# Kernel optimization log

Hardware: AMD Instinct MI355X
Metric: run time of the kernel (lower is better)

The kernel has to match this reference:

```python
import jax, jax.numpy as jnp
import numpy as np

N_HEADS = 16
HEAD_DIM = 64
HIDDEN = 1024


def setup_inputs() -> dict:
    key = jax.random.key(0)
    kx, kq, kk, kv, ko = jax.random.split(key, 5)
    B, S = 1, 4096
    # xavier_uniform for Linear(hidden, n_heads*head_dim): limit = sqrt(6/(fan_in+fan_out))
    lim = float(np.sqrt(6.0 / (HIDDEN + N_HEADS * HEAD_DIM)))
    x = jax.random.normal(kx, (B, S, HIDDEN), dtype=jnp.float32)
    wq = jax.random.uniform(kq, (N_HEADS * HEAD_DIM, HIDDEN), jnp.float32, -lim, lim)
    wk = jax.random.uniform(kk, (N_HEADS * HEAD_DIM, HIDDEN), jnp.float32, -lim, lim)
    wv = jax.random.uniform(kv, (N_HEADS * HEAD_DIM, HIDDEN), jnp.float32, -lim, lim)
    wo = jax.random.uniform(ko, (HIDDEN, N_HEADS * HEAD_DIM), jnp.float32, -lim, lim)
    return {"x": x, "wq": wq, "wk": wk, "wv": wv, "wo": wo}


def reference(x, wq, wk, wv, wo):
    B, S, _ = x.shape
    scale = HEAD_DIM ** -0.5
    # project and split heads: [B, H, S, D]
    def proj(w):
        return jnp.einsum('bsh,eh->bse', x, w).reshape(B, S, N_HEADS, HEAD_DIM).transpose(0, 2, 1, 3)
    q, k, v = proj(wq), proj(wk), proj(wv)
    scores = jnp.einsum('bhqd,bhkd->bhqk', q, k) * scale  # [B,H,S,S]
    causal = jnp.tril(jnp.ones((S, S), dtype=bool))
    scores = jnp.where(causal, scores, -jnp.inf)
    probs = jax.nn.softmax(scores, axis=-1)
    out = jnp.einsum('bhqk,bhkd->bhqd', probs, v)  # [B,H,S,D]
    out = out.transpose(0, 2, 1, 3).reshape(B, S, N_HEADS * HEAD_DIM)
    return jnp.einsum('bse,he->bsh', out, wo)
```

## Files before the change

### kernel.cpp

```cpp
#include <hip/hip_runtime.h>
#include <hip/hip_bf16.h>
#include <stdint.h>

typedef unsigned short u16;
typedef float f32x4 __attribute__((ext_vector_type(4)));
typedef __bf16 bf16x8 __attribute__((ext_vector_type(8)));
typedef u16 u16x8 __attribute__((ext_vector_type(8)));

#define GL2LDS16(g, l)                                                          \
  __builtin_amdgcn_global_load_lds(                                             \
      (const __attribute__((address_space(1))) unsigned int*)(g),               \
      (__attribute__((address_space(3))) unsigned int*)(l), 16, 0, 0)

#if __has_builtin(__builtin_amdgcn_exp2f)
#define EXP2(x) __builtin_amdgcn_exp2f(x)
#else
#define EXP2(x) exp2f(x)
#endif

#define SOFTMAX_SC 0.18033688f

__device__ __forceinline__ u16 f2bf(float f) {
  uint32_t u = __builtin_bit_cast(uint32_t, f);
  return (u16)((u + 0x7FFFu + ((u >> 16) & 1u)) >> 16);
}

__device__ __forceinline__ uint32_t cvt_pk_bf16(float lo, float hi) {
  uint32_t r;
  asm("v_cvt_pk_bf16_f32 %0, %1, %2" : "=v"(r) : "v"(lo), "v"(hi));
  return r;
}

__device__ __forceinline__ void cast8(const float* __restrict__ s,
                                      u16* __restrict__ d) {
  const float4* p = (const float4*)s;
  float4 a = p[0], b = p[1];
  uint4 o;
  o.x = cvt_pk_bf16(a.x, a.y);
  o.y = cvt_pk_bf16(a.z, a.w);
  o.z = cvt_pk_bf16(b.x, b.y);
  o.w = cvt_pk_bf16(b.z, b.w);
  *(uint4*)d = o;
}

__global__ __launch_bounds__(256) void cast_kernel(const float* __restrict__ s,
                                                   u16* __restrict__ d, int n) {
  int i = (blockIdx.x * 256 + threadIdx.x) * 8;
  if (i >= n) return;
  cast8(s + i, d + i);
}

__global__ __launch_bounds__(256) void cast4_kernel(const float* __restrict__ s0,
                                                    const float* __restrict__ s1,
                                                    const float* __restrict__ s2,
                                                    const float* __restrict__ s3,
                                                    u16* __restrict__ d) {
  int b = blockIdx.x >> 9;
  int i = ((blockIdx.x & 511) * 256 + threadIdx.x) * 8;
  const float* s = (b == 0) ? s0 : (b == 1) ? s1 : (b == 2) ? s2 : s3;
  cast8(s + i, d + ((size_t)b << 20) + i);
}

template <int MB>
__device__ __forceinline__ void mfma16(f32x4 (&acc)[8][4], const bf16x8 (&af)[4],
                                       const bf16x8 (&bfr)[4]) {
  asm volatile("s_waitcnt lgkmcnt(0)" ::: "memory");
  __builtin_amdgcn_sched_barrier(0);
  __builtin_amdgcn_s_setprio(1);
#pragma unroll
  for (int j = 0; j < 4; ++j)
#pragma unroll
    for (int n = 0; n < 4; ++n)
      acc[MB + j][n] = __builtin_amdgcn_mfma_f32_16x16x32_bf16(
          af[j], bfr[n], acc[MB + j][n], 0, 0, 0);
  __builtin_amdgcn_s_setprio(0);
}

__global__ __launch_bounds__(512, 2) void gemm8k(const u16* __restrict__ A,
                                                 const u16* __restrict__ B,
                                                 u16* __restrict__ C, int M,
                                                 int N, int K, int scaleq) {
  __shared__ u16 As[4][128 * 64];
  __shared__ u16 Bs[4][128 * 64];
  const int tid = threadIdx.x;
  const int lane = tid & 63;
  const int l15 = lane & 15, lhi = lane >> 4;
  const int wave = tid >> 6;
  const int wm = wave >> 2, wn = wave & 3;
  int bid = blockIdx.y * gridDim.x + blockIdx.x;
  const int cpx = (gridDim.x * gridDim.y) >> 3;
  bid = (bid & 7) * cpx + (bid >> 3);
  const int m0 = (bid / gridDim.x) * 256, n0 = (bid % gridDim.x) * 256;
  const int nt = K >> 6;

  int aoff[2][8], boff[2][4];
#pragma unroll
  for (int ks = 0; ks < 2; ++ks) {
    const int sl = ((ks * 4 + lhi) ^ (l15 & 7)) << 4;
#pragma unroll
    for (int m = 0; m < 8; ++m) aoff[ks][m] = (m * 16 + l15) * 128 + sl;
#pragma unroll
    for (int n = 0; n < 4; ++n)
      boff[ks][n] = ((wn & 1) * 64 + n * 16 + l15) * 128 + sl;
  }

  auto stA = [&](int T, int h) {
    u16* lb = As[(T & 1) * 2 + h];
#pragma unroll
    for (int i = 0; i < 2; ++i) {
      int c = tid + i * 512;
      int row = c >> 3;
      int scol = ((c & 7) ^ (row & 7)) * 8;
      GL2LDS16(A + (size_t)(m0 + h * 128 + row) * K + T * 64 + scol,
               (char*)lb + c * 16);
    }
  };
  auto stB = [&](int T, int h) {
    u16* lb = Bs[(T & 1) * 2 + h];
#pragma unroll
    for (int i = 0; i < 2; ++i) {
      int c = tid + i * 512;
      int row = c >> 3;
      int scol = ((c & 7) ^ (row & 7)) * 8;
      GL2LDS16(B + (size_t)(n0 + h * 128 + row) * K + T * 64 + scol,
               (char*)lb + c * 16);
    }
  };

  f32x4 acc[8][4] = {};

  stA(0, 0); stA(0, 1); stB(0, 0); stB(0, 1);
  asm volatile("s_waitcnt vmcnt(0)" ::: "memory");
  __builtin_amdgcn_s_barrier();

  for (int i = 0; i < nt / 2; ++i) {
    const int e = 2 * i, o = e + 1;
    const char* Ae = (const char*)As[wm];
    const char* Be = (const char*)Bs[wn >> 1];
    const char* Ao = (const char*)As[2 + wm];
    const char* Bo = (const char*)Bs[2 + (wn >> 1)];
    bf16x8 af[4], bfr[4];
    const bool pre = (e + 2) < nt;

    stA(o, 0); stA(o, 1);
    asm volatile("s_waitcnt vmcnt(4)" ::: "memory");
    __builtin_amdgcn_s_barrier();
#pragma unroll
    for (int j = 0; j < 4; ++j) af[j] = *(const bf16x8*)(Ae + aoff[0][j]);
#pragma unroll
    for (int n = 0; n < 4; ++n) bfr[n] = *(const bf16x8*)(Be + boff[0][n]);
    mfma16<0>(acc, af, bfr);
    __builtin_amdgcn_s_barrier();
#pragma unroll
    for (int j = 0; j < 4; ++j) af[j] = *(const bf16x8*)(Ae + aoff[0][4 + j]);
    stB(o, 0); stB(o, 1);
    __builtin_amdgcn_s_barrier();
    mfma16<4>(acc, af, bfr);
    __builtin_amdgcn_s_barrier();
#pragma unroll
    for (int j = 0; j < 4; ++j) af[j] = *(const bf16x8*)(Ae + aoff[1][j]);
#pragma unroll
    for (int n = 0; n < 4; ++n) bfr[n] = *(const bf16x8*)(Be + boff[1][n]);
    __builtin_amdgcn_s_barrier();
    mfma16<0>(acc, af, bfr);
    __builtin_amdgcn_s_barrier();
#pragma unroll
    for (int j = 0; j < 4; ++j) af[j] = *(const bf16x8*)(Ae + aoff[1][4 + j]);
    __builtin_amdgcn_s_barrier();
    mfma16<4>(acc, af, bfr);
    __builtin_amdgcn_s_barrier();
    if (pre) {
      stA(e + 2, 0); stA(e + 2, 1);
      asm volatile("s_waitcnt vmcnt(4)" ::: "memory");
    } else {
      asm volatile("s_waitcnt vmcnt(0)" ::: "memory");
    }
    __builtin_amdgcn_s_barrier();
#pragma unroll
    for (int j = 0; j < 4; ++j) af[j] = *(const bf16x8*)(Ao + aoff[0][j]);
#pragma unroll
    for (int n = 0; n < 4; ++n) bfr[n] = *(const bf16x8*)(Bo + boff[0][n]);
    mfma16<0>(acc, af, bfr);
    __builtin_amdgcn_s_barrier();
#pragma unroll
    for (int j = 0; j < 4; ++j) af[j] = *(const bf16x8*)(Ao + aoff[0][4 + j]);
    if (pre) { stB(e + 2, 0); stB(e + 2, 1); }
    __builtin_amdgcn_s_barrier();
    mfma16<4>(acc, af, bfr);
    __builtin_amdgcn_s_barrier();
#pragma unroll
    for (int j = 0; j < 4; ++j) af[j] = *(const bf16x8*)(Ao + aoff[1][j]);
#pragma unroll
    for (int n = 0; n < 4; ++n) bfr[n] = *(const bf16x8*)(Bo + boff[1][n]);
    __builtin_amdgcn_s_barrier();
    mfma16<0>(acc, af, bfr);
    __builtin_amdgcn_s_barrier();
#pragma unroll
    for (int j = 0; j < 4; ++j) af[j] = *(const bf16x8*)(Ao + aoff[1][4 + j]);
    __builtin_amdgcn_s_barrier();
    mfma16<4>(acc, af, bfr);
    __builtin_amdgcn_s_barrier();
  }

#pragma unroll
  for (int m = 0; m < 8; ++m) {
    int rbase = m0 + wm * 128 + m * 16 + lhi * 4;
#pragma unroll
    for (int n = 0; n < 4; ++n) {
      int col = n0 + wn * 64 + n * 16 + l15;
      float sc = (scaleq && col < 1024) ? SOFTMAX_SC : 1.0f;
#pragma unroll
      for (int r = 0; r < 4; ++r)
        C[(size_t)(rbase + r) * N + col] = f2bf(acc[m][n][r] * sc);
    }
  }
}

template <typename CT>
__global__ __launch_bounds__(256) void gemm_bt(const u16* __restrict__ A,
                                               const u16* __restrict__ B,
                                               CT* __restrict__ C, int M, int N,
                                               int K) {
  __shared__ u16 As[128 * 32];
  __shared__ u16 Bs[128 * 32];
  const int tid = threadIdx.x;
  const int lane = tid & 63;
  const int l15 = lane & 15, lhi = lane >> 4;
  const int wave = tid >> 6;
  const int wr = (wave >> 1) * 64, wc = (wave & 1) * 64;
  const int m0 = blockIdx.y * 128, n0 = blockIdx.x * 128;

  f32x4 acc[4][4] = {};

  for (int k0 = 0; k0 < K; k0 += 32) {
    __syncthreads();
#pragma unroll
    for (int i = 0; i < 2; ++i) {
      int c = tid + i * 256;
      int row = c >> 2, slot = c & 3;
      int scol = (slot ^ ((row >> 1) & 3)) * 8;
      GL2LDS16(A + (size_t)(m0 + row) * K + k0 + scol, (char*)As + c * 16);
      GL2LDS16(B + (size_t)(n0 + row) * K + k0 + scol, (char*)Bs + c * 16);
    }
    __syncthreads();
    bf16x8 af[4], bfr[4];
#pragma unroll
    for (int mi = 0; mi < 4; ++mi) {
      int row = wr + mi * 16 + l15;
      int byt = row * 64 + ((lhi ^ ((row >> 1) & 3)) << 4);
      af[mi] = *(const bf16x8*)((const char*)As + byt);
    }
#pragma unroll
    for (int ni = 0; ni < 4; ++ni) {
      int row = wc + ni * 16 + l15;
      int byt = row * 64 + ((lhi ^ ((row >> 1) & 3)) << 4);
      bfr[ni] = *(const bf16x8*)((const char*)Bs + byt);
    }
#pragma unroll
    for (int mi = 0; mi < 4; ++mi)
#pragma unroll
      for (int ni = 0; ni < 4; ++ni)
        acc[mi][ni] = __builtin_amdgcn_mfma_f32_16x16x32_bf16(
            af[mi], bfr[ni], acc[mi][ni], 0, 0, 0);
  }

#pragma unroll
  for (int mi = 0; mi < 4; ++mi) {
    int rbase = m0 + wr + mi * 16 + lhi * 4;
#pragma unroll
    for (int ni = 0; ni < 4; ++ni) {
      int col = n0 + wc + ni * 16 + l15;
#pragma unroll
      for (int r = 0; r < 4; ++r) {
        float v = acc[mi][ni][r];
        if constexpr (sizeof(CT) == 2)
          C[(size_t)(rbase + r) * N + col] = (CT)f2bf(v);
        else
          C[(size_t)(rbase + r) * N + col] = v;
      }
    }
  }
}

__global__ __launch_bounds__(256) void vtrans_kernel(const u16* __restrict__ qkv,
                                                     u16* __restrict__ vt) {
  __shared__ u16 t[64][72];
  const int bs = blockIdx.x * 64;
  const int be = blockIdx.y * 64;
  const int tid = threadIdx.x;
#pragma unroll
  for (int i = 0; i < 2; ++i) {
    int c = tid + i * 256, row = c >> 3, col = (c & 7) * 8;
    *(u16x8*)&t[row][col] =
        *(const u16x8*)(qkv + (size_t)(bs + row) * 3072 + 2048 + be + col);
  }
  __syncthreads();
#pragma unroll
  for (int i = 0; i < 2; ++i) {
    int c = tid + i * 256, erow = c >> 3, scol = (c & 7) * 8;
    u16x8 o;
#pragma unroll
    for (int j = 0; j < 8; ++j) o[j] = t[scol + j][erow];
    *(u16x8*)(vt + (size_t)(be + erow) * 4096 + bs + scol) = o;
  }
}

__global__ __launch_bounds__(512) void attn_kernel(const u16* __restrict__ qkv,
                                                   const u16* __restrict__ vt,
                                                   u16* __restrict__ out) {
  const int h = blockIdx.y;
  const int bx = blockIdx.x;
  const int tid = threadIdx.x;
  const int lane = tid & 63, wave = tid >> 6;
  const int l15 = lane & 15, lhi = lane >> 4;

  __shared__ u16 Ks[2][64 * 64];
  __shared__ u16 Vs[2][64 * 64];
  __shared__ u16 Ps[8][16 * 64];
  u16* Pw = Ps[wave];

  int koff[2][4];
#pragma unroll
  for (int ks = 0; ks < 2; ++ks)
#pragma unroll
    for (int nf = 0; nf < 4; ++nf) {
      int row = nf * 16 + l15;
      koff[ks][nf] = row * 128 + ((lhi * 16 + ks * 64) ^ ((row & 7) << 4));
    }
  int poff[4];
#pragma unroll
  for (int nf = 0; nf < 4; ++nf)
    poff[nf] = l15 * 128 + ((nf * 32 + lhi * 8) ^ ((l15 & 7) << 4));

  auto stage = [&](int b, int kb) {
    int c = tid;
    int row = c >> 3, slot = c & 7;
    int scol = (slot ^ (row & 7)) * 8;
    GL2LDS16(qkv + (size_t)(kb * 64 + row) * 3072 + 1024 + h * 64 + scol,
             (char*)(Ks[b]) + c * 16);
    GL2LDS16(vt + (size_t)(h * 64 + row) * 4096 + kb * 64 + scol,
             (char*)(Vs[b]) + c * 16);
  };

  int cur = 0;
  for (int rep = 0; rep < 2; ++rep) {
    const int qsb = rep ? (31 - bx) : bx;
    const int ntile = 2 * qsb + 2;
    const int q0 = qsb * 128 + wave * 16;
    const u16* Qb = qkv + (size_t)(q0 + l15) * 3072 + h * 64;
    bf16x8 qf0 = *(const bf16x8*)(const void*)(Qb + lhi * 8);
    bf16x8 qf1 = *(const bf16x8*)(const void*)(Qb + 32 + lhi * 8);

    f32x4 oa[4] = {};
    float mrow = -1e30f, lrow = 0.f;

    stage(cur, 0);
    asm volatile("s_waitcnt vmcnt(0)" ::: "memory");
    __builtin_amdgcn_s_barrier();

    for (int kb = 0; kb < ntile; ++kb) {
      if (kb + 1 < ntile) stage(cur ^ 1, kb + 1);

      f32x4 s[4] = {};
#pragma unroll
      for (int ks = 0; ks < 2; ++ks)
#pragma unroll
        for (int nf = 0; nf < 4; ++nf) {
          bf16x8 kf =
              *(const bf16x8*)((const char*)(Ks[cur]) + koff[ks][nf]);
          s[nf] = __builtin_amdgcn_mfma_f32_16x16x32_bf16(kf, ks ? qf1 : qf0,
                                                          s[nf], 0, 0, 0);
        }

      if (kb * 64 + 63 > q0) {
        const int q = q0 + l15;
#pragma unroll
        for (int nf = 0; nf < 4; ++nf)
#pragma unroll
          for (int r = 0; r < 4; ++r)
            if (kb * 64 + nf * 16 + lhi * 4 + r > q) s[nf][r] = -1e30f;
      }

      float pm0 = fmaxf(fmaxf(s[0][0], s[0][1]), fmaxf(s[0][2], s[0][3]));
      float pm1 = fmaxf(fmaxf(s[1][0], s[1][1]), fmaxf(s[1][2], s[1][3]));
      float pm2 = fmaxf(fmaxf(s[2][0], s[2][1]), fmaxf(s[2][2], s[2][3]));
      float pm3 = fmaxf(fmaxf(s[3][0], s[3][1]), fmaxf(s[3][2], s[3][3]));
      float pm = fmaxf(fmaxf(pm0, pm1), fmaxf(pm2, pm3));
      pm = fmaxf(pm, __shfl_xor(pm, 16));
      pm = fmaxf(pm, __shfl_xor(pm, 32));

      if (__any(pm - mrow > 8.0f)) {
        float mn = fmaxf(mrow, pm);
        float al = EXP2(mrow - mn);
        mrow = mn;
        lrow *= al;
        float alq[4];
#pragma unroll
        for (int r = 0; r < 4; ++r) alq[r] = __shfl(al, lhi * 4 + r, 16);
#pragma unroll
        for (int nf = 0; nf < 4; ++nf)
#pragma unroll
          for (int r = 0; r < 4; ++r) oa[nf][r] *= alq[r];
      }

#pragma unroll
      for (int nf = 0; nf < 4; ++nf)
#pragma unroll
        for (int r = 0; r < 4; ++r) s[nf][r] = EXP2(s[nf][r] - mrow);
      float rs = ((s[0][0] + s[0][1]) + (s[0][2] + s[0][3])) +
                 ((s[1][0] + s[1][1]) + (s[1][2] + s[1][3])) +
                 ((s[2][0] + s[2][1]) + (s[2][2] + s[2][3])) +
                 ((s[3][0] + s[3][1]) + (s[3][2] + s[3][3]));
      rs += __shfl_xor(rs, 16);
      rs += __shfl_xor(rs, 32);
      lrow += rs;

#pragma unroll
      for (int nf = 0; nf < 4; ++nf) {
        uint2 pk;
        pk.x = cvt_pk_bf16(s[nf][0], s[nf][1]);
        pk.y = cvt_pk_bf16(s[nf][2], s[nf][3]);
        *(uint2*)((char*)Pw + poff[nf]) = pk;
      }

      bf16x8 pf[2];
#pragma unroll
      for (int ks = 0; ks < 2; ++ks)
        pf[ks] = *(const bf16x8*)((const char*)Pw + koff[ks][0]);

#pragma unroll
      for (int ks = 0; ks < 2; ++ks)
#pragma unroll
        for (int nf = 0; nf < 4; ++nf) {
          bf16x8 vf =
              *(const bf16x8*)((const char*)(Vs[cur]) + koff[ks][nf]);
          oa[nf] = __builtin_amdgcn_mfma_f32_16x16x32_bf16(pf[ks], vf, oa[nf],
                                                           0, 0, 0);
        }

      asm volatile("s_waitcnt vmcnt(0)" ::: "memory");
      __builtin_amdgcn_s_barrier();
      cur ^= 1;
    }

    float linv[4];
#pragma unroll
    for (int r = 0; r < 4; ++r)
      linv[r] = 1.0f / __shfl(lrow, lhi * 4 + r, 16);
#pragma unroll
    for (int r = 0; r < 4; ++r) {
      int rowg = q0 + lhi * 4 + r;
#pragma unroll
      for (int nf = 0; nf < 4; ++nf)
        out[(size_t)rowg * 1024 + h * 64 + nf * 16 + l15] =
            f2bf(oa[nf][r] * linv[r]);
    }
  }
}

extern "C" void kernel_launch(void* const* d_in, const int* in_sizes, int n_in,
                              void* d_out, int out_size, void* d_ws,
                              size_t ws_size, hipStream_t stream) {
  const float* x = (const float*)d_in[0];
  const float* wq = (const float*)d_in[1];
  const float* wk = (const float*)d_in[2];
  const float* wv = (const float*)d_in[3];
  const float* wo = (const float*)d_in[4];

  u16* xb = (u16*)d_ws;
  u16* wqkv = xb + 4096 * 1024;
  u16* wob = wqkv + 3072 * 1024;
  u16* qkv = wob + 1024 * 1024;
  u16* atn = qkv + (size_t)4096 * 3072;
  u16* vt = xb;

  cast_kernel<<<2048, 256, 0, stream>>>(x, xb, 4096 * 1024);
  cast4_kernel<<<2048, 256, 0, stream>>>(wq, wk, wv, wo, wqkv);

  gemm8k<<<dim3(12, 16), 512, 0, stream>>>(xb, wqkv, qkv, 4096, 3072, 1024, 1);
  vtrans_kernel<<<dim3(64, 16), 256, 0, stream>>>(qkv, vt);
  attn_kernel<<<dim3(16, 16), 512, 0, stream>>>(qkv, vt, atn);
  gemm_bt<float><<<dim3(8, 32), 256, 0, stream>>>(atn, wob, (float*)d_out, 4096,
                                                  1024, 1024);
}
```

Measured before the change: 238.7 us.

## Split attention key range into two halves and merge partials afterwards

Adds a third grid dimension that splits each query block's causal key range into two halves, doubling the number of attention workgroups. Each half writes a normalized partial output plus per-row max and sum. A new merge kernel rescales and combines the two partials into the final attention output. The aim is more parallelism and better CU occupancy, at the cost of extra memory traffic and a kernel launch. Rows with no unmasked keys in one half depend on how the masked path handles its sentinel values.

```diff
diff --git a/kernel.cpp b/kernel.cpp
--- a/kernel.cpp
+++ b/kernel.cpp
@@ -23,6 +23,10 @@
 __device__ __forceinline__ u16 f2bf(float f) {
   uint32_t u = __builtin_bit_cast(uint32_t, f);
   return (u16)((u + 0x7FFFu + ((u >> 16) & 1u)) >> 16);
+}
+
+__device__ __forceinline__ float bf2f(u16 b) {
+  return __builtin_bit_cast(float, (uint32_t)b << 16);
 }
 
 __device__ __forceinline__ uint32_t cvt_pk_bf16(float lo, float hi) {
@@ -307,12 +311,17 @@
 
 __global__ __launch_bounds__(512) void attn_kernel(const u16* __restrict__ qkv,
                                                    const u16* __restrict__ vt,
-                                                   u16* __restrict__ out) {
+                                                   u16* __restrict__ pout,
+                                                   float2* __restrict__ mlb) {
   const int h = blockIdx.y;
   const int bx = blockIdx.x;
+  const int half = blockIdx.z;
   const int tid = threadIdx.x;
   const int lane = tid & 63, wave = tid >> 6;
   const int l15 = lane & 15, lhi = lane >> 4;
+
+  u16* po = pout + (size_t)half * 4096 * 1024;
+  float2* ml = mlb + (size_t)half * 4096 * 16;
 
   __shared__ u16 Ks[2][64 * 64];
   __shared__ u16 Vs[2][64 * 64];
@@ -345,7 +354,8 @@
   int cur = 0;
   for (int rep = 0; rep < 2; ++rep) {
     const int qsb = rep ? (31 - bx) : bx;
-    const int ntile = 2 * qsb + 2;
+    const int kb0 = half * (qsb + 1);
+    const int kbe = kb0 + qsb + 1;
     const int q0 = qsb * 128 + wave * 16;
     const u16* Qb = qkv + (size_t)(q0 + l15) * 3072 + h * 64;
     bf16x8 qf0 = *(const bf16x8*)(const void*)(Qb + lhi * 8);
@@ -354,12 +364,12 @@
     f32x4 oa[4] = {};
     float mrow = -1e30f, lrow = 0.f;
 
-    stage(cur, 0);
+    stage(cur, kb0);
     asm volatile("s_waitcnt vmcnt(0)" ::: "memory");
     __builtin_amdgcn_s_barrier();
 
-    for (int kb = 0; kb < ntile; ++kb) {
-      if (kb + 1 < ntile) stage(cur ^ 1, kb + 1);
+    for (int kb = kb0; kb < kbe; ++kb) {
+      if (kb + 1 < kbe) stage(cur ^ 1, kb + 1);
 
       f32x4 s[4] = {};
 #pragma unroll
@@ -452,10 +462,30 @@
       int rowg = q0 + lhi * 4 + r;
 #pragma unroll
       for (int nf = 0; nf < 4; ++nf)
-        out[(size_t)rowg * 1024 + h * 64 + nf * 16 + l15] =
+        po[(size_t)rowg * 1024 + h * 64 + nf * 16 + l15] =
             f2bf(oa[nf][r] * linv[r]);
     }
-  }
+    if (lhi == 0) ml[(q0 + l15) * 16 + h] = float2{mrow, lrow};
+  }
+}
+
+__global__ __launch_bounds__(256) void merge_kernel(const u16* __restrict__ po,
+                                                    const float2* __restrict__ mlb,
+                                                    u16* __restrict__ atn) {
+  int base = (blockIdx.x * 256 + threadIdx.x) * 8;
+  int row = base >> 10, h = (base & 1023) >> 6;
+  float2 a = mlb[row * 16 + h];
+  float2 b = mlb[4096 * 16 + row * 16 + h];
+  float m = fmaxf(a.x, b.x);
+  float w0 = EXP2(a.x - m) * a.y, w1 = EXP2(b.x - m) * b.y;
+  float inv = 1.0f / (w0 + w1);
+  w0 *= inv; w1 *= inv;
+  u16x8 p0 = *(const u16x8*)(po + base);
+  u16x8 p1 = *(const u16x8*)(po + 4096 * 1024 + base);
+  u16x8 o;
+#pragma unroll
+  for (int j = 0; j < 8; ++j) o[j] = f2bf(w0 * bf2f(p0[j]) + w1 * bf2f(p1[j]));
+  *(u16x8*)(atn + base) = o;
 }
 
 extern "C" void kernel_launch(void* const* d_in, const int* in_sizes, int n_in,
@@ -473,13 +503,16 @@
   u16* qkv = wob + 1024 * 1024;
   u16* atn = qkv + (size_t)4096 * 3072;
   u16* vt = xb;
+  float2* mlb = (float2*)wqkv;
+  u16* pout = (u16*)d_out;
 
   cast_kernel<<<2048, 256, 0, stream>>>(x, xb, 4096 * 1024);
   cast4_kernel<<<2048, 256, 0, stream>>>(wq, wk, wv, wo, wqkv);
 
   gemm8k<<<dim3(12, 16), 512, 0, stream>>>(xb, wqkv, qkv, 4096, 3072, 1024, 1);
   vtrans_kernel<<<dim3(64, 16), 256, 0, stream>>>(qkv, vt);
-  attn_kernel<<<dim3(16, 16), 512, 0, stream>>>(qkv, vt, atn);
+  attn_kernel<<<dim3(16, 16, 2), 512, 0, stream>>>(qkv, vt, pout, mlb);
+  merge_kernel<<<2048, 256, 0, stream>>>(pout, mlb, atn);
   gemm_bt<float><<<dim3(8, 32), 256, 0, stream>>>(atn, wob, (float*)d_out, 4096,
                                                   1024, 1024);
 }
```

New measurement: 219.9 us. -7.9%, faster.
